# Performance work log

Measured on AMD Instinct MI355X. Metric: run time of the kernel, lower is better.

Reference implementation:

```python
import jax, jax.numpy as jnp
import numpy as np
import math

B, N, DQK, DV, M = 8, 8192, 128, 128, 256


def _make_omega(m: int, d: int, seed: int = 0) -> jnp.ndarray:
    """Block-orthogonal random feature matrix, shape [d, m] (matches torch _omega)."""
    rng = np.random.default_rng(seed)
    blocks = []
    nblocks = m // d
    for _ in range(nblocks):
        q, _ = np.linalg.qr(rng.standard_normal((d, d)))
        blocks.append(q.T)
    missing = m - nblocks * d
    if missing > 0:
        q, _ = np.linalg.qr(rng.standard_normal((d, d)))
        blocks.append(q.T[:missing])
    norm = np.linalg.norm(rng.standard_normal((m, d)), axis=1, keepdims=True)
    omega = (norm * np.vstack(blocks)).T  # [d, m]
    return jnp.asarray(omega, dtype=jnp.float32)


def setup_inputs() -> dict:
    key = jax.random.key(0)
    kq, kk, kv = jax.random.split(key, 3)
    Q = jax.random.normal(kq, (B, N, DQK), jnp.float32)
    K = jax.random.normal(kk, (B, N, DQK), jnp.float32)
    V = jax.random.normal(kv, (B, N, DV), jnp.float32)
    atom_mask = jnp.ones((B, N), jnp.float32)
    omega = _make_omega(M, DQK)
    return {"Q": Q, "K": K, "V": V, "atom_mask": atom_mask, "omega": omega}


def _phi(X, mask, omega, is_query: bool, eps: float = 1e-4):
    """Project into random-feature space with Performer stabilization."""
    d = X.shape[-1]
    m = omega.shape[-1]
    U = (X / d ** 0.25) @ omega                       # [B, N, m]
    h = jnp.sum(X * X, axis=-1, keepdims=True) / (2.0 * d ** 0.5)
    if is_query:
        mx = jnp.max(U, axis=-1, keepdims=True)       # per-token max
    else:
        mx = jnp.max(U, axis=(-2, -1), keepdims=True)  # per-batch max
    return (jnp.exp(U - h - mx) + eps) / math.sqrt(m) * mask[..., None]


def reference(Q, K, V, atom_mask, omega):
    eps = 1e-8
    Qp = _phi(Q, atom_mask, omega, True)   # [B, N, M]
    Kp = _phi(K, atom_mask, omega, False)  # [B, N, M]
    # norm_n = Qp_n . sum_j Kp_j
    norm = jnp.einsum('bnm,bm->bn', Qp, jnp.sum(Kp, axis=1))[..., None] + eps
    KV = jnp.einsum('bnm,bnv->bmv', Kp, V)             # [B, M, DV]
    return jnp.einsum('bnm,bmv->bnv', Qp, KV) / norm   # [B, N, DV]
```

## Files before the change

kernel.cpp:

```cpp
#include <hip/hip_runtime.h>
#include <math.h>

#define BB 8
#define NN 8192
#define DD 128
#define MM 256
#define DVV 128
#define PP 32
#define CHUNK 32

#define XSCALE 0.29730177875068026f
#define INV_SQRT_M 0.0625f

typedef _Float16 f16x8 __attribute__((ext_vector_type(8)));
typedef float f32x16 __attribute__((ext_vector_type(16)));

#define FR(s, l) ((s) * 520 + (l) * 8)

__device__ __forceinline__ unsigned f2ord(float f) {
    unsigned u = __float_as_uint(f);
    return (u & 0x80000000u) ? ~u : (u | 0x80000000u);
}
__device__ __forceinline__ float ord2f(unsigned u) {
    return (u & 0x80000000u) ? __uint_as_float(u & 0x7fffffffu) : __uint_as_float(~u);
}
__device__ __forceinline__ f32x16 mfma16(f16x8 a, f16x8 b, f32x16 c) {
    return __builtin_amdgcn_mfma_f32_32x32x16_f16(a, b, c, 0, 0, 0);
}
__device__ __forceinline__ int rowf(int r, int q) { return (r & 3) + 8 * (r >> 2) + 4 * q; }

__device__ __forceinline__ void stage_A(const float* __restrict__ src,
                                        _Float16* R1, float* hs, float* msk,
                                        const float* __restrict__ mrow, bool do_h) {
    const int tid = threadIdx.x;
    const int t = tid >> 3, ks = tid & 7;
    const float4* s4 = (const float4*)(src + t * DD + ks * 16);
    float x[16];
    #pragma unroll
    for (int u = 0; u < 4; ++u) {
        float4 v = s4[u];
        x[u*4+0] = v.x * XSCALE; x[u*4+1] = v.y * XSCALE;
        x[u*4+2] = v.z * XSCALE; x[u*4+3] = v.w * XSCALE;
    }
    if (do_h) {
        float p = 0.f;
        #pragma unroll
        for (int u = 0; u < 16; ++u) p += x[u] * x[u];
        p += __shfl_xor(p, 1, 64); p += __shfl_xor(p, 2, 64); p += __shfl_xor(p, 4, 64);
        if (ks == 0) { hs[t] = 0.5f * p; msk[t] = mrow[t]; }
    }
    #pragma unroll
    for (int q = 0; q < 2; ++q) {
        f16x8 h8, l8;
        #pragma unroll
        for (int j = 0; j < 8; ++j) {
            float xv = x[q*8 + j];
            _Float16 h = (_Float16)xv;
            h8[j] = h; l8[j] = (_Float16)(xv - (float)h);
        }
        *(f16x8*)&R1[FR(0*8 + ks, q*32 + t)] = h8;
        *(f16x8*)&R1[FR(1*8 + ks, q*32 + t)] = l8;
    }
}

__device__ __forceinline__ void stage_BV(const float* __restrict__ src, _Float16* R1) {
    const int tid = threadIdx.x;
    const int t = tid >> 3, c0 = (tid & 7) * 16;
    const int ts = t >> 4, qq = (t >> 3) & 1, j = t & 7;
    const float4* s4 = (const float4*)(src + t * DVV + c0);
    #pragma unroll
    for (int u = 0; u < 4; ++u) {
        float4 v = s4[u];
        float vv[4] = {v.x, v.y, v.z, v.w};
        #pragma unroll
        for (int e = 0; e < 4; ++e) {
            int c = c0 + u*4 + e;
            int vt = c >> 5, iv = c & 31;
            _Float16 h = (_Float16)vv[e];
            R1[FR((0*4 + vt)*2 + ts, qq*32 + iv) + j] = h;
            R1[FR((1*4 + vt)*2 + ts, qq*32 + iv) + j] = (_Float16)(vv[e] - (float)h);
        }
    }
}

__global__ __launch_bounds__(256) void pack_kernel(const float* __restrict__ omega,
                                                   _Float16* __restrict__ omh,
                                                   _Float16* __restrict__ oml,
                                                   unsigned* __restrict__ kmaxord) {
    int g = blockIdx.x * 256 + threadIdx.x;
    if (g < BB) kmaxord[g] = f2ord(-INFINITY);
    int lane = g & 63, ks = (g >> 6) & 7, nt = g >> 9;
    int q = lane >> 5, i = lane & 31;
    f16x8 h8, l8;
    #pragma unroll
    for (int j = 0; j < 8; ++j) {
        float w = omega[(size_t)(ks*16 + q*8 + j) * MM + nt*32 + i];
        _Float16 h = (_Float16)w;
        h8[j] = h; l8[j] = (_Float16)(w - (float)h);
    }
    ((f16x8*)omh)[g] = h8;
    ((f16x8*)oml)[g] = l8;
}

__global__ __launch_bounds__(256) void kmax_kernel(const float* __restrict__ K,
                                                   const _Float16* __restrict__ omh,
                                                   unsigned* __restrict__ kmaxord) {
    __shared__ __align__(16) _Float16 R1[16 * 520];
    __shared__ float wred[4];
    const int b = blockIdx.y;
    const int tid = threadIdx.x, w = tid >> 6, lane = tid & 63;
    const int w2 = 2 * w;
    const f16x8* OH = (const f16x8*)omh;

    float mx = -INFINITY;
    #pragma unroll 1
    for (int c = 0; c < 2; ++c) {
        int t0 = (blockIdx.x * 2 + c) * CHUNK;
        __syncthreads();
        stage_A(K + ((size_t)b*NN + t0) * DD, R1, nullptr, nullptr, nullptr, false);
        __syncthreads();
        f32x16 a0, a1;
        #pragma unroll
        for (int r = 0; r < 16; ++r) { a0[r] = 0.f; a1[r] = 0.f; }
        f16x8 X0 = OH[(w2*8 + 0)*64 + lane];
        f16x8 X1 = OH[((w2+1)*8 + 0)*64 + lane];
        #pragma unroll 1
        for (int ks = 0; ks < 8; ks += 2) {
            f16x8 Y0 = OH[(w2*8 + ks + 1)*64 + lane];
            f16x8 Y1 = OH[((w2+1)*8 + ks + 1)*64 + lane];
            f16x8 ah = *(const f16x8*)&R1[FR(ks, lane)];
            a0 = mfma16(ah, X0, a0);
            a1 = mfma16(ah, X1, a1);
            int k2 = (ks + 2) & 7;
            X0 = OH[(w2*8 + k2)*64 + lane];
            X1 = OH[((w2+1)*8 + k2)*64 + lane];
            f16x8 ah2 = *(const f16x8*)&R1[FR(ks + 1, lane)];
            a0 = mfma16(ah2, Y0, a0);
            a1 = mfma16(ah2, Y1, a1);
        }
        #pragma unroll
        for (int r = 0; r < 16; ++r) mx = fmaxf(mx, fmaxf(a0[r], a1[r]));
    }
    #pragma unroll
    for (int off = 1; off < 64; off <<= 1) mx = fmaxf(mx, __shfl_xor(mx, off, 64));
    if (lane == 0) wred[w] = mx;
    __syncthreads();
    if (tid == 0)
        atomicMax(kmaxord + b,
                  f2ord(fmaxf(fmaxf(wred[0], wred[1]), fmaxf(wred[2], wred[3]))));
}

__global__ __launch_bounds__(256) void kv_kernel(const float* __restrict__ K,
                                                 const float* __restrict__ V,
                                                 const float* __restrict__ mask,
                                                 const _Float16* __restrict__ omh,
                                                 const _Float16* __restrict__ oml,
                                                 const unsigned* __restrict__ kmaxord,
                                                 float* __restrict__ pkv,
                                                 float* __restrict__ pks) {
    __shared__ __align__(16) _Float16 R1[16 * 520];
    __shared__ __align__(16) _Float16 R2[16 * 520];
    __shared__ float hs[32], msk[32];
    const int b = blockIdx.y, bx = blockIdx.x;
    const int rest = bx >> 3;
    const int h = rest & 1;
    const int p = (rest >> 1) * 8 + (bx & 7);
    const int tid = threadIdx.x, w = tid >> 6, lane = tid & 63;
    const int i = tid & 31, q = (tid >> 5) & 1;
    const int nt = h * 4 + w;
    const float kmaxv = ord2f(kmaxord[b]);
    const f16x8* OH = (const f16x8*)omh;
    const f16x8* OL = (const f16x8*)oml;

    f32x16 kvacc[4];
    #pragma unroll
    for (int vt = 0; vt < 4; ++vt)
        #pragma unroll
        for (int r = 0; r < 16; ++r) kvacc[vt][r] = 0.f;
    float ksa = 0.f;

    #pragma unroll 1
    for (int c = 0; c < 8; ++c) {
        int t0 = (p * 8 + c) * CHUNK;
        __syncthreads();
        stage_A(K + ((size_t)b*NN + t0) * DD, R1, hs, msk,
                mask + (size_t)b*NN + t0, true);
        __syncthreads();

        f32x16 a0;
        #pragma unroll
        for (int r = 0; r < 16; ++r) a0[r] = 0.f;
        f16x8 Xh = OH[(nt*8 + 0)*64 + lane];
        f16x8 Xl = OL[(nt*8 + 0)*64 + lane];
        #pragma unroll 1
        for (int ks = 0; ks < 8; ks += 2) {
            f16x8 Yh = OH[(nt*8 + ks + 1)*64 + lane];
            f16x8 Yl = OL[(nt*8 + ks + 1)*64 + lane];
            f16x8 ah = *(const f16x8*)&R1[FR(ks, lane)];
            f16x8 al = *(const f16x8*)&R1[FR(8 + ks, lane)];
            a0 = mfma16(ah, Xh, a0);
            a0 = mfma16(ah, Xl, a0);
            a0 = mfma16(al, Xh, a0);
            int k2 = (ks + 2) & 7;
            Xh = OH[(nt*8 + k2)*64 + lane];
            Xl = OL[(nt*8 + k2)*64 + lane];
            f16x8 ah2 = *(const f16x8*)&R1[FR(ks + 1, lane)];
            f16x8 al2 = *(const f16x8*)&R1[FR(8 + ks + 1, lane)];
            a0 = mfma16(ah2, Yh, a0);
            a0 = mfma16(ah2, Yl, a0);
            a0 = mfma16(al2, Yh, a0);
        }
        __syncthreads();

        stage_BV(V + ((size_t)b*NN + t0) * DVV, R1);
        #pragma unroll
        for (int r = 0; r < 16; ++r) {
            int tok = rowf(r, q);
            float hh = hs[tok] + kmaxv;
            float mm = msk[tok] * INV_SQRT_M;
            float kp = (__expf(a0[r] - hh) + 1e-4f) * mm;
            ksa += kp;
            int ts = tok >> 4, qq = (tok >> 3) & 1, j = tok & 7;
            _Float16 hv = (_Float16)kp;
            R2[FR(w*2 + ts, qq*32 + i) + j] = hv;
            R2[FR(8 + w*2 + ts, qq*32 + i) + j] = (_Float16)(kp - (float)hv);
        }
        __syncthreads();

        f16x8 ah2[2], al2[2];
        #pragma unroll
        for (int ts = 0; ts < 2; ++ts) {
            ah2[ts] = *(const f16x8*)&R2[FR(w*2 + ts, lane)];
            al2[ts] = *(const f16x8*)&R2[FR(8 + w*2 + ts, lane)];
        }
        #pragma unroll
        for (int vt = 0; vt < 4; ++vt) {
            #pragma unroll
            for (int ts = 0; ts < 2; ++ts) {
                f16x8 bh = *(const f16x8*)&R1[FR(vt*2 + ts, lane)];
                f16x8 bl = *(const f16x8*)&R1[FR(8 + vt*2 + ts, lane)];
                kvacc[vt] = mfma16(ah2[ts], bh, kvacc[vt]);
                kvacc[vt] = mfma16(ah2[ts], bl, kvacc[vt]);
                kvacc[vt] = mfma16(al2[ts], bh, kvacc[vt]);
            }
        }
    }

    float* dst = pkv + ((size_t)(b * PP + p) << 15);
    #pragma unroll
    for (int vt = 0; vt < 4; ++vt)
        #pragma unroll
        for (int r = 0; r < 16; ++r) {
            int feat = nt*32 + rowf(r, q);
            dst[feat * DVV + vt*32 + i] = kvacc[vt][r];
        }
    {
        float s = ksa + __shfl_xor(ksa, 32, 64);
        if (q == 0) pks[(size_t)(b * PP + p) * MM + nt*32 + i] = s;
    }
}

__global__ __launch_bounds__(256) void reduce_kernel(const float* __restrict__ pkv,
                                                     const float* __restrict__ pks,
                                                     float* __restrict__ ksum,
                                                     _Float16* __restrict__ kvph,
                                                     _Float16* __restrict__ kvpl) {
    const int b = blockIdx.y;
    int g = blockIdx.x * 256 + threadIdx.x;
    float s = 0.f;
    for (int p = 0; p < PP; ++p) s += pkv[((size_t)(b * PP + p) << 15) + g];
    int f = g >> 7, v = g & 127;
    int vt = v >> 5, iv = v & 31, fs = f >> 4, qq = (f >> 3) & 1, j = f & 7;
    size_t idx = (size_t)b * 32768 + (size_t)((vt*16 + fs)*64 + qq*32 + iv)*8 + j;
    _Float16 h = (_Float16)s;
    kvph[idx] = h;
    kvpl[idx] = (_Float16)(s - (float)h);
    if (blockIdx.x == 0) {
        float ss = 0.f;
        for (int p = 0; p < PP; ++p) ss += pks[(size_t)(b * PP + p) * MM + g];
        ksum[b * MM + g] = ss;
    }
}

__global__ __launch_bounds__(256) void out_kernel(const float* __restrict__ Q,
                                                  const float* __restrict__ mask,
                                                  const _Float16* __restrict__ omh,
                                                  const _Float16* __restrict__ oml,
                                                  const float* __restrict__ ksum,
                                                  const _Float16* __restrict__ kvph,
                                                  const _Float16* __restrict__ kvpl,
                                                  float* __restrict__ out) {
    __shared__ __align__(16) _Float16 R2[32 * 520];
    __shared__ float hs[32], msk[32], wmax[4][32], norms[32];
    const int b = blockIdx.y;
    const int tid = threadIdx.x, w = tid >> 6, lane = tid & 63;
    const int i = tid & 31, q = (tid >> 5) & 1;
    const int w2 = 2 * w;
    const f16x8* OH = (const f16x8*)omh;
    const f16x8* OL = (const f16x8*)oml;
    const f16x8* KH = (const f16x8*)kvph + (size_t)b * 4096 + (w*16)*64 + lane;
    const f16x8* KL = (const f16x8*)kvpl + (size_t)b * 4096 + (w*16)*64 + lane;
    const float nk0 = ksum[b * MM + w2*32 + i];
    const float nk1 = ksum[b * MM + (w2+1)*32 + i];

    #pragma unroll 1
    for (int c = 0; c < 2; ++c) {
        int t0 = (blockIdx.x * 2 + c) * CHUNK;
        __syncthreads();
        stage_A(Q + ((size_t)b*NN + t0) * DD, R2, hs, msk,
                mask + (size_t)b*NN + t0, true);
        if (tid < 32) norms[tid] = 1e-8f;
        __syncthreads();

        f32x16 a0, a1;
        #pragma unroll
        for (int r = 0; r < 16; ++r) { a0[r] = 0.f; a1[r] = 0.f; }
        f16x8 X0h = OH[(w2*8 + 0)*64 + lane], X0l = OL[(w2*8 + 0)*64 + lane];
        f16x8 X1h = OH[((w2+1)*8 + 0)*64 + lane], X1l = OL[((w2+1)*8 + 0)*64 + lane];
        #pragma unroll 1
        for (int ks = 0; ks < 8; ks += 2) {
            f16x8 Y0h = OH[(w2*8 + ks + 1)*64 + lane], Y0l = OL[(w2*8 + ks + 1)*64 + lane];
            f16x8 Y1h = OH[((w2+1)*8 + ks + 1)*64 + lane], Y1l = OL[((w2+1)*8 + ks + 1)*64 + lane];
            f16x8 ah = *(const f16x8*)&R2[FR(ks, lane)];
            f16x8 al = *(const f16x8*)&R2[FR(8 + ks, lane)];
            a0 = mfma16(ah, X0h, a0); a0 = mfma16(ah, X0l, a0); a0 = mfma16(al, X0h, a0);
            a1 = mfma16(ah, X1h, a1); a1 = mfma16(ah, X1l, a1); a1 = mfma16(al, X1h, a1);
            int k2 = (ks + 2) & 7;
            X0h = OH[(w2*8 + k2)*64 + lane]; X0l = OL[(w2*8 + k2)*64 + lane];
            X1h = OH[((w2+1)*8 + k2)*64 + lane]; X1l = OL[((w2+1)*8 + k2)*64 + lane];
            f16x8 ah2 = *(const f16x8*)&R2[FR(ks + 1, lane)];
            f16x8 al2 = *(const f16x8*)&R2[FR(8 + ks + 1, lane)];
            a0 = mfma16(ah2, Y0h, a0); a0 = mfma16(ah2, Y0l, a0); a0 = mfma16(al2, Y0h, a0);
            a1 = mfma16(ah2, Y1h, a1); a1 = mfma16(ah2, Y1l, a1); a1 = mfma16(al2, Y1h, a1);
        }

        float tm[16];
        #pragma unroll
        for (int r = 0; r < 16; ++r) tm[r] = fmaxf(a0[r], a1[r]);
        #pragma unroll
        for (int off = 1; off < 32; off <<= 1)
            #pragma unroll
            for (int r = 0; r < 16; ++r) tm[r] = fmaxf(tm[r], __shfl_xor(tm[r], off, 64));
        if (i == 0)
            #pragma unroll
            for (int r = 0; r < 16; ++r) wmax[w][rowf(r, q)] = tm[r];
        __syncthreads();

        float nacc[16];
        #pragma unroll
        for (int r = 0; r < 16; ++r) {
            int tok = rowf(r, q);
            float tmax = fmaxf(fmaxf(wmax[0][tok], wmax[1][tok]),
                               fmaxf(wmax[2][tok], wmax[3][tok]));
            float hh = hs[tok] + tmax;
            float mm = msk[tok] * INV_SQRT_M;
            float qp0 = (__expf(a0[r] - hh) + 1e-4f) * mm;
            float qp1 = (__expf(a1[r] - hh) + 1e-4f) * mm;
            nacc[r] = qp0 * nk0 + qp1 * nk1;
            {
                int feat = w2*32 + i;
                int fstep = feat >> 4, fq = (i >> 3) & 1, fj = i & 7;
                _Float16 hv = (_Float16)qp0;
                R2[FR(fstep, fq*32 + tok) + fj] = hv;
                R2[FR(16 + fstep, fq*32 + tok) + fj] = (_Float16)(qp0 - (float)hv);
            }
            {
                int feat = (w2+1)*32 + i;
                int fstep = feat >> 4, fq = (i >> 3) & 1, fj = i & 7;
                _Float16 hv = (_Float16)qp1;
                R2[FR(fstep, fq*32 + tok) + fj] = hv;
                R2[FR(16 + fstep, fq*32 + tok) + fj] = (_Float16)(qp1 - (float)hv);
            }
        }
        #pragma unroll
        for (int off = 1; off < 32; off <<= 1)
            #pragma unroll
            for (int r = 0; r < 16; ++r) nacc[r] += __shfl_xor(nacc[r], off, 64);
        if (i == 0)
            #pragma unroll
            for (int r = 0; r < 16; ++r) atomicAdd(&norms[rowf(r, q)], nacc[r]);
        __syncthreads();

        f32x16 oa;
        #pragma unroll
        for (int r = 0; r < 16; ++r) oa[r] = 0.f;
        f16x8 Fh = KH[0], Fl = KL[0];
        #pragma unroll 1
        for (int fs = 0; fs < 16; fs += 2) {
            f16x8 Gh = KH[(fs + 1)*64], Gl = KL[(fs + 1)*64];
            f16x8 ah = *(const f16x8*)&R2[FR(fs, lane)];
            f16x8 al = *(const f16x8*)&R2[FR(16 + fs, lane)];
            oa = mfma16(ah, Fh, oa); oa = mfma16(ah, Fl, oa); oa = mfma16(al, Fh, oa);
            int f2 = (fs + 2) & 15;
            Fh = KH[f2*64]; Fl = KL[f2*64];
            f16x8 ah2 = *(const f16x8*)&R2[FR(fs + 1, lane)];
            f16x8 al2 = *(const f16x8*)&R2[FR(16 + fs + 1, lane)];
            oa = mfma16(ah2, Gh, oa); oa = mfma16(ah2, Gl, oa); oa = mfma16(al2, Gh, oa);
        }

        float* ob = out + ((size_t)b*NN + t0) * DVV + w*32 + i;
        #pragma unroll
        for (int r = 0; r < 16; ++r) {
            int tok = rowf(r, q);
            ob[(size_t)tok * DVV] = oa[r] * __builtin_amdgcn_rcpf(norms[tok]);
        }
    }
}

extern "C" void kernel_launch(void* const* d_in, const int* in_sizes, int n_in,
                              void* d_out, int out_size, void* d_ws, size_t ws_size,
                              hipStream_t stream) {
    const float* Q     = (const float*)d_in[0];
    const float* K     = (const float*)d_in[1];
    const float* V     = (const float*)d_in[2];
    const float* mask  = (const float*)d_in[3];
    const float* omega = (const float*)d_in[4];
    float* out = (float*)d_out;

    char* ws = (char*)d_ws;
    _Float16* omh    = (_Float16*)(ws);
    _Float16* oml    = (_Float16*)(ws + (64 << 10));
    unsigned* kmaxord = (unsigned*)(ws + (128 << 10));
    float*    ksum   = (float*)(ws + (132 << 10));
    float*    pks    = (float*)(ws + (140 << 10));
    _Float16* kvph   = (_Float16*)(ws + (400 << 10));
    _Float16* kvpl   = (_Float16*)(ws + (912 << 10));
    float*    pkv    = (float*)(ws + (2 << 20));

    pack_kernel<<<16, 256, 0, stream>>>(omega, omh, oml, kmaxord);
    kmax_kernel<<<dim3(128, BB), 256, 0, stream>>>(K, omh, kmaxord);
    kv_kernel<<<dim3(64, BB), 256, 0, stream>>>(K, V, mask, omh, oml, kmaxord, pkv, pks);
    reduce_kernel<<<dim3(128, BB), 256, 0, stream>>>(pkv, pks, ksum, kvph, kvpl);
    out_kernel<<<dim3(128, BB), 256, 0, stream>>>(Q, mask, omh, oml, ksum, kvph, kvpl, out);
}
```

Before: 250.8 us.

## Software-pipeline kv and out kernels with register prefetch and double-buffered LDS

The kv kernel now prefetches the next chunk's K, V and mask into registers while computing the current chunk. It overlaps the previous chunk's KV MFMA accumulation with the current projection, using double-buffered V tiles and h/mask arrays. The out kernel is restructured the same way: the next chunk's Q is prefetched, the previous chunk's PV product is interleaved with the current projection, and norm atomics are replaced by per-wave shared partials. The grid is halved so each block handles four chunks, and the inner loops are fully unrolled. The changes aim to hide global load latency and cut barriers, at the cost of more LDS and register pressure, which may lower occupancy.

```diff
diff --git a/kernel.cpp b/kernel.cpp
--- a/kernel.cpp
+++ b/kernel.cpp
@@ -29,57 +29,55 @@
 }
 __device__ __forceinline__ int rowf(int r, int q) { return (r & 3) + 8 * (r >> 2) + 4 * q; }
 
-__device__ __forceinline__ void stage_A(const float* __restrict__ src,
-                                        _Float16* R1, float* hs, float* msk,
-                                        const float* __restrict__ mrow, bool do_h) {
+__device__ __forceinline__ void loadX16(const float* __restrict__ src, float x[16]) {
+    const int tid = threadIdx.x;
+    const float4* s4 = (const float4*)(src + (tid >> 3) * 128 + (tid & 7) * 16);
+    #pragma unroll
+    for (int u = 0; u < 4; ++u) {
+        float4 v = s4[u];
+        x[u*4+0] = v.x; x[u*4+1] = v.y; x[u*4+2] = v.z; x[u*4+3] = v.w;
+    }
+}
+
+__device__ __forceinline__ void writeA(const float xin[16], _Float16* R1,
+                                       float* hs, float* msk, float mv, bool do_h) {
     const int tid = threadIdx.x;
     const int t = tid >> 3, ks = tid & 7;
-    const float4* s4 = (const float4*)(src + t * DD + ks * 16);
     float x[16];
     #pragma unroll
-    for (int u = 0; u < 4; ++u) {
-        float4 v = s4[u];
-        x[u*4+0] = v.x * XSCALE; x[u*4+1] = v.y * XSCALE;
-        x[u*4+2] = v.z * XSCALE; x[u*4+3] = v.w * XSCALE;
-    }
+    for (int u = 0; u < 16; ++u) x[u] = xin[u] * XSCALE;
     if (do_h) {
         float p = 0.f;
         #pragma unroll
         for (int u = 0; u < 16; ++u) p += x[u] * x[u];
         p += __shfl_xor(p, 1, 64); p += __shfl_xor(p, 2, 64); p += __shfl_xor(p, 4, 64);
-        if (ks == 0) { hs[t] = 0.5f * p; msk[t] = mrow[t]; }
-    }
-    #pragma unroll
-    for (int q = 0; q < 2; ++q) {
+        if (ks == 0) { hs[t] = 0.5f * p; msk[t] = mv; }
+    }
+    #pragma unroll
+    for (int qq = 0; qq < 2; ++qq) {
         f16x8 h8, l8;
         #pragma unroll
         for (int j = 0; j < 8; ++j) {
-            float xv = x[q*8 + j];
+            float xv = x[qq*8 + j];
             _Float16 h = (_Float16)xv;
             h8[j] = h; l8[j] = (_Float16)(xv - (float)h);
         }
-        *(f16x8*)&R1[FR(0*8 + ks, q*32 + t)] = h8;
-        *(f16x8*)&R1[FR(1*8 + ks, q*32 + t)] = l8;
-    }
-}
-
-__device__ __forceinline__ void stage_BV(const float* __restrict__ src, _Float16* R1) {
+        *(f16x8*)&R1[FR(0*8 + ks, qq*32 + t)] = h8;
+        *(f16x8*)&R1[FR(1*8 + ks, qq*32 + t)] = l8;
+    }
+}
+
+__device__ __forceinline__ void writeV(const float xin[16], _Float16* RV) {
     const int tid = threadIdx.x;
     const int t = tid >> 3, c0 = (tid & 7) * 16;
     const int ts = t >> 4, qq = (t >> 3) & 1, j = t & 7;
-    const float4* s4 = (const float4*)(src + t * DVV + c0);
-    #pragma unroll
-    for (int u = 0; u < 4; ++u) {
-        float4 v = s4[u];
-        float vv[4] = {v.x, v.y, v.z, v.w};
-        #pragma unroll
-        for (int e = 0; e < 4; ++e) {
-            int c = c0 + u*4 + e;
-            int vt = c >> 5, iv = c & 31;
-            _Float16 h = (_Float16)vv[e];
-            R1[FR((0*4 + vt)*2 + ts, qq*32 + iv) + j] = h;
-            R1[FR((1*4 + vt)*2 + ts, qq*32 + iv) + j] = (_Float16)(vv[e] - (float)h);
-        }
+    #pragma unroll
+    for (int u = 0; u < 16; ++u) {
+        int c = c0 + u;
+        int vt = c >> 5, iv = c & 31;
+        _Float16 h = (_Float16)xin[u];
+        RV[FR((0*4 + vt)*2 + ts, qq*32 + iv) + j] = h;
+        RV[FR((1*4 + vt)*2 + ts, qq*32 + iv) + j] = (_Float16)(xin[u] - (float)h);
     }
 }
 
@@ -117,26 +115,25 @@
     for (int c = 0; c < 2; ++c) {
         int t0 = (blockIdx.x * 2 + c) * CHUNK;
         __syncthreads();
-        stage_A(K + ((size_t)b*NN + t0) * DD, R1, nullptr, nullptr, nullptr, false);
+        {
+            float xk[16];
+            loadX16(K + ((size_t)b*NN + t0) * DD, xk);
+            writeA(xk, R1, nullptr, nullptr, 0.f, false);
+        }
         __syncthreads();
         f32x16 a0, a1;
         #pragma unroll
         for (int r = 0; r < 16; ++r) { a0[r] = 0.f; a1[r] = 0.f; }
         f16x8 X0 = OH[(w2*8 + 0)*64 + lane];
         f16x8 X1 = OH[((w2+1)*8 + 0)*64 + lane];
-        #pragma unroll 1
-        for (int ks = 0; ks < 8; ks += 2) {
-            f16x8 Y0 = OH[(w2*8 + ks + 1)*64 + lane];
-            f16x8 Y1 = OH[((w2+1)*8 + ks + 1)*64 + lane];
+        #pragma unroll
+        for (int ks = 0; ks < 8; ++ks) {
+            f16x8 Y0, Y1;
+            if (ks < 7) { Y0 = OH[(w2*8 + ks + 1)*64 + lane]; Y1 = OH[((w2+1)*8 + ks + 1)*64 + lane]; }
             f16x8 ah = *(const f16x8*)&R1[FR(ks, lane)];
             a0 = mfma16(ah, X0, a0);
             a1 = mfma16(ah, X1, a1);
-            int k2 = (ks + 2) & 7;
-            X0 = OH[(w2*8 + k2)*64 + lane];
-            X1 = OH[((w2+1)*8 + k2)*64 + lane];
-            f16x8 ah2 = *(const f16x8*)&R1[FR(ks + 1, lane)];
-            a0 = mfma16(ah2, Y0, a0);
-            a1 = mfma16(ah2, Y1, a1);
+            X0 = Y0; X1 = Y1;
         }
         #pragma unroll
         for (int r = 0; r < 16; ++r) mx = fmaxf(mx, fmaxf(a0[r], a1[r]));
@@ -160,7 +157,9 @@
                                                  float* __restrict__ pks) {
     __shared__ __align__(16) _Float16 R1[16 * 520];
     __shared__ __align__(16) _Float16 R2[16 * 520];
-    __shared__ float hs[32], msk[32];
+    __shared__ __align__(16) _Float16 RV0[16 * 520];
+    __shared__ __align__(16) _Float16 RV1[16 * 520];
+    __shared__ float hs[2][32], msk[2][32];
     const int b = blockIdx.y, bx = blockIdx.x;
     const int rest = bx >> 3;
     const int h = rest & 1;
@@ -168,9 +167,13 @@
     const int tid = threadIdx.x, w = tid >> 6, lane = tid & 63;
     const int i = tid & 31, q = (tid >> 5) & 1;
     const int nt = h * 4 + w;
+    const int tld = tid >> 3;
     const float kmaxv = ord2f(kmaxord[b]);
     const f16x8* OH = (const f16x8*)omh;
     const f16x8* OL = (const f16x8*)oml;
+    const float* Kb = K + (size_t)b * NN * DD;
+    const float* Vb = V + (size_t)b * NN * DVV;
+    const float* Mb = mask + (size_t)b * NN;
 
     f32x16 kvacc[4];
     #pragma unroll
@@ -179,46 +182,77 @@
         for (int r = 0; r < 16; ++r) kvacc[vt][r] = 0.f;
     float ksa = 0.f;
 
+    {
+        int t0 = p * 8 * CHUNK;
+        float xk[16], xv[16];
+        loadX16(Kb + (size_t)t0 * DD, xk);
+        loadX16(Vb + (size_t)t0 * DVV, xv);
+        float mv = Mb[t0 + tld];
+        writeA(xk, R1, hs[0], msk[0], mv, true);
+        writeV(xv, RV0);
+    }
+    __syncthreads();
+
     #pragma unroll 1
-    for (int c = 0; c < 8; ++c) {
-        int t0 = (p * 8 + c) * CHUNK;
-        __syncthreads();
-        stage_A(K + ((size_t)b*NN + t0) * DD, R1, hs, msk,
-                mask + (size_t)b*NN + t0, true);
-        __syncthreads();
-
-        f32x16 a0;
-        #pragma unroll
-        for (int r = 0; r < 16; ++r) a0[r] = 0.f;
+    for (int t = 0; t < 8; ++t) {
+        const bool pre = (t + 1 < 8);
+        float xk[16], xv[16], mv = 0.f;
+        if (pre) {
+            int t1 = (p * 8 + t + 1) * CHUNK;
+            loadX16(Kb + (size_t)t1 * DD, xk);
+            loadX16(Vb + (size_t)t1 * DVV, xv);
+            mv = Mb[t1 + tld];
+        }
+        _Float16* RVprev = (t & 1) ? RV0 : RV1;
+
+        f32x16 a0a, a0b;
+        #pragma unroll
+        for (int r = 0; r < 16; ++r) { a0a[r] = 0.f; a0b[r] = 0.f; }
+        f16x8 kh0, kl0, kh1, kl1;
+        if (t > 0) {
+            kh0 = *(const f16x8*)&R2[FR(w*2 + 0, lane)];
+            kl0 = *(const f16x8*)&R2[FR(8 + w*2 + 0, lane)];
+            kh1 = *(const f16x8*)&R2[FR(w*2 + 1, lane)];
+            kl1 = *(const f16x8*)&R2[FR(8 + w*2 + 1, lane)];
+        }
         f16x8 Xh = OH[(nt*8 + 0)*64 + lane];
         f16x8 Xl = OL[(nt*8 + 0)*64 + lane];
-        #pragma unroll 1
-        for (int ks = 0; ks < 8; ks += 2) {
-            f16x8 Yh = OH[(nt*8 + ks + 1)*64 + lane];
-            f16x8 Yl = OL[(nt*8 + ks + 1)*64 + lane];
-            f16x8 ah = *(const f16x8*)&R1[FR(ks, lane)];
-            f16x8 al = *(const f16x8*)&R1[FR(8 + ks, lane)];
-            a0 = mfma16(ah, Xh, a0);
-            a0 = mfma16(ah, Xl, a0);
-            a0 = mfma16(al, Xh, a0);
-            int k2 = (ks + 2) & 7;
-            Xh = OH[(nt*8 + k2)*64 + lane];
-            Xl = OL[(nt*8 + k2)*64 + lane];
-            f16x8 ah2 = *(const f16x8*)&R1[FR(ks + 1, lane)];
-            f16x8 al2 = *(const f16x8*)&R1[FR(8 + ks + 1, lane)];
-            a0 = mfma16(ah2, Yh, a0);
-            a0 = mfma16(ah2, Yl, a0);
-            a0 = mfma16(al2, Yh, a0);
+        #pragma unroll
+        for (int s = 0; s < 8; ++s) {
+            f16x8 Yh, Yl;
+            if (s < 7) { Yh = OH[(nt*8 + s + 1)*64 + lane]; Yl = OL[(nt*8 + s + 1)*64 + lane]; }
+            f16x8 ah = *(const f16x8*)&R1[FR(s, lane)];
+            f16x8 al = *(const f16x8*)&R1[FR(8 + s, lane)];
+            if (s & 1) {
+                a0b = mfma16(ah, Xh, a0b); a0b = mfma16(ah, Xl, a0b); a0b = mfma16(al, Xh, a0b);
+            } else {
+                a0a = mfma16(ah, Xh, a0a); a0a = mfma16(ah, Xl, a0a); a0a = mfma16(al, Xh, a0a);
+            }
+            if (t > 0) {
+                const int vt = s >> 1, ts = s & 1;
+                f16x8 kh = ts ? kh1 : kh0, kl = ts ? kl1 : kl0;
+                f16x8 bh = *(const f16x8*)&RVprev[FR(vt*2 + ts, lane)];
+                f16x8 bl = *(const f16x8*)&RVprev[FR(8 + vt*2 + ts, lane)];
+                kvacc[vt] = mfma16(kh, bh, kvacc[vt]);
+                kvacc[vt] = mfma16(kh, bl, kvacc[vt]);
+                kvacc[vt] = mfma16(kl, bh, kvacc[vt]);
+            }
+            Xh = Yh; Xl = Yl;
         }
         __syncthreads();
 
-        stage_BV(V + ((size_t)b*NN + t0) * DVV, R1);
+        if (pre) {
+            writeA(xk, R1, hs[(t+1)&1], msk[(t+1)&1], mv, true);
+            writeV(xv, RVprev);
+        }
+        const float* hsv = hs[t & 1];
+        const float* mskv = msk[t & 1];
         #pragma unroll
         for (int r = 0; r < 16; ++r) {
             int tok = rowf(r, q);
-            float hh = hs[tok] + kmaxv;
-            float mm = msk[tok] * INV_SQRT_M;
-            float kp = (__expf(a0[r] - hh) + 1e-4f) * mm;
+            float hh = hsv[tok] + kmaxv;
+            float mm = mskv[tok] * INV_SQRT_M;
+            float kp = (__expf((a0a[r] + a0b[r]) - hh) + 1e-4f) * mm;
             ksa += kp;
             int ts = tok >> 4, qq = (tok >> 3) & 1, j = tok & 7;
             _Float16 hv = (_Float16)kp;
@@ -226,22 +260,23 @@
             R2[FR(8 + w*2 + ts, qq*32 + i) + j] = (_Float16)(kp - (float)hv);
         }
         __syncthreads();
-
-        f16x8 ah2[2], al2[2];
-        #pragma unroll
-        for (int ts = 0; ts < 2; ++ts) {
-            ah2[ts] = *(const f16x8*)&R2[FR(w*2 + ts, lane)];
-            al2[ts] = *(const f16x8*)&R2[FR(8 + w*2 + ts, lane)];
-        }
+    }
+
+    {
+        f16x8 kh0 = *(const f16x8*)&R2[FR(w*2 + 0, lane)];
+        f16x8 kl0 = *(const f16x8*)&R2[FR(8 + w*2 + 0, lane)];
+        f16x8 kh1 = *(const f16x8*)&R2[FR(w*2 + 1, lane)];
+        f16x8 kl1 = *(const f16x8*)&R2[FR(8 + w*2 + 1, lane)];
         #pragma unroll
         for (int vt = 0; vt < 4; ++vt) {
             #pragma unroll
             for (int ts = 0; ts < 2; ++ts) {
-                f16x8 bh = *(const f16x8*)&R1[FR(vt*2 + ts, lane)];
-                f16x8 bl = *(const f16x8*)&R1[FR(8 + vt*2 + ts, lane)];
-                kvacc[vt] = mfma16(ah2[ts], bh, kvacc[vt]);
-                kvacc[vt] = mfma16(ah2[ts], bl, kvacc[vt]);
-                kvacc[vt] = mfma16(al2[ts], bh, kvacc[vt]);
+                f16x8 kh = ts ? kh1 : kh0, kl = ts ? kl1 : kl0;
+                f16x8 bh = *(const f16x8*)&RV1[FR(vt*2 + ts, lane)];
+                f16x8 bl = *(const f16x8*)&RV1[FR(8 + vt*2 + ts, lane)];
+                kvacc[vt] = mfma16(kh, bh, kvacc[vt]);
+                kvacc[vt] = mfma16(kh, bl, kvacc[vt]);
+                kvacc[vt] = mfma16(kl, bh, kvacc[vt]);
             }
         }
     }
@@ -290,120 +325,151 @@
                                                   const _Float16* __restrict__ kvph,
                                                   const _Float16* __restrict__ kvpl,
                                                   float* __restrict__ out) {
+    __shared__ __align__(16) _Float16 R1[16 * 520];
     __shared__ __align__(16) _Float16 R2[32 * 520];
-    __shared__ float hs[32], msk[32], wmax[4][32], norms[32];
+    __shared__ float hs[2][32], msk[2][32], wmax[4][32], nws[2][4][32];
     const int b = blockIdx.y;
     const int tid = threadIdx.x, w = tid >> 6, lane = tid & 63;
     const int i = tid & 31, q = (tid >> 5) & 1;
     const int w2 = 2 * w;
+    const int tld = tid >> 3;
     const f16x8* OH = (const f16x8*)omh;
     const f16x8* OL = (const f16x8*)oml;
     const f16x8* KH = (const f16x8*)kvph + (size_t)b * 4096 + (w*16)*64 + lane;
     const f16x8* KL = (const f16x8*)kvpl + (size_t)b * 4096 + (w*16)*64 + lane;
     const float nk0 = ksum[b * MM + w2*32 + i];
     const float nk1 = ksum[b * MM + (w2+1)*32 + i];
+    const float* Qb = Q + (size_t)b * NN * DD;
+    const float* Mb = mask + (size_t)b * NN;
+    const int base = blockIdx.x * 4;
+
+    {
+        float xq[16];
+        loadX16(Qb + (size_t)(base * CHUNK) * DD, xq);
+        float mv = Mb[base * CHUNK + tld];
+        writeA(xq, R1, hs[0], msk[0], mv, true);
+    }
+    __syncthreads();
 
     #pragma unroll 1
-    for (int c = 0; c < 2; ++c) {
-        int t0 = (blockIdx.x * 2 + c) * CHUNK;
+    for (int c = 0; c < 5; ++c) {
+        const bool doU  = (c < 4);
+        const bool doPV = (c > 0);
+        const bool pre  = (c + 1 < 4);
+        float xq[16], mv = 0.f;
+        if (pre) {
+            int t1 = (base + c + 1) * CHUNK;
+            loadX16(Qb + (size_t)t1 * DD, xq);
+            mv = Mb[t1 + tld];
+        }
+
+        f32x16 a0, a1, oa, ob;
+        #pragma unroll
+        for (int r = 0; r < 16; ++r) { a0[r] = 0.f; a1[r] = 0.f; oa[r] = 0.f; ob[r] = 0.f; }
+        f16x8 X0h, X0l, X1h, X1l, F0h, F0l, F1h, F1l;
+        if (doU) {
+            X0h = OH[(w2*8 + 0)*64 + lane];     X0l = OL[(w2*8 + 0)*64 + lane];
+            X1h = OH[((w2+1)*8 + 0)*64 + lane]; X1l = OL[((w2+1)*8 + 0)*64 + lane];
+        }
+        if (doPV) {
+            F0h = KH[0*64]; F0l = KL[0*64];
+            F1h = KH[1*64]; F1l = KL[1*64];
+        }
+        #pragma unroll
+        for (int s = 0; s < 8; ++s) {
+            f16x8 Y0h, Y0l, Y1h, Y1l, G0h, G0l, G1h, G1l;
+            if (s < 7) {
+                if (doU) {
+                    Y0h = OH[(w2*8 + s + 1)*64 + lane];     Y0l = OL[(w2*8 + s + 1)*64 + lane];
+                    Y1h = OH[((w2+1)*8 + s + 1)*64 + lane]; Y1l = OL[((w2+1)*8 + s + 1)*64 + lane];
+                }
+                if (doPV) {
+                    G0h = KH[(2*s + 2)*64]; G0l = KL[(2*s + 2)*64];
+                    G1h = KH[(2*s + 3)*64]; G1l = KL[(2*s + 3)*64];
+                }
+            }
+            if (doU) {
+                f16x8 ah = *(const f16x8*)&R1[FR(s, lane)];
+                f16x8 al = *(const f16x8*)&R1[FR(8 + s, lane)];
+                a0 = mfma16(ah, X0h, a0); a0 = mfma16(ah, X0l, a0); a0 = mfma16(al, X0h, a0);
+                a1 = mfma16(ah, X1h, a1); a1 = mfma16(ah, X1l, a1); a1 = mfma16(al, X1h, a1);
+            }
+            if (doPV) {
+                f16x8 ph0 = *(const f16x8*)&R2[FR(2*s, lane)];
+                f16x8 pl0 = *(const f16x8*)&R2[FR(16 + 2*s, lane)];
+                oa = mfma16(ph0, F0h, oa); oa = mfma16(ph0, F0l, oa); oa = mfma16(pl0, F0h, oa);
+                f16x8 ph1 = *(const f16x8*)&R2[FR(2*s + 1, lane)];
+                f16x8 pl1 = *(const f16x8*)&R2[FR(16 + 2*s + 1, lane)];
+                ob = mfma16(ph1, F1h, ob); ob = mfma16(ph1, F1l, ob); ob = mfma16(pl1, F1h, ob);
+            }
+            X0h = Y0h; X0l = Y0l; X1h = Y1h; X1l = Y1l;
+            F0h = G0h; F0l = G0l; F1h = G1h; F1l = G1l;
+        }
+
+        if (doPV) {
+            const int pb = (c - 1) & 1;
+            int tp = (base + c - 1) * CHUNK;
+            float* obp = out + ((size_t)b*NN + tp) * DVV + w*32 + i;
+            #pragma unroll
+            for (int r = 0; r < 16; ++r) {
+                int tok = rowf(r, q);
+                float nrm = nws[pb][0][tok] + nws[pb][1][tok]
+                          + nws[pb][2][tok] + nws[pb][3][tok] + 1e-8f;
+                obp[(size_t)tok * DVV] = (oa[r] + ob[r]) * __builtin_amdgcn_rcpf(nrm);
+            }
+        }
+
+        if (doU) {
+            float tm[16];
+            #pragma unroll
+            for (int r = 0; r < 16; ++r) tm[r] = fmaxf(a0[r], a1[r]);
+            #pragma unroll
+            for (int off = 1; off < 32; off <<= 1)
+                #pragma unroll
+                for (int r = 0; r < 16; ++r) tm[r] = fmaxf(tm[r], __shfl_xor(tm[r], off, 64));
+            if (i == 0)
+                #pragma unroll
+                for (int r = 0; r < 16; ++r) wmax[w][rowf(r, q)] = tm[r];
+        }
         __syncthreads();
-        stage_A(Q + ((size_t)b*NN + t0) * DD, R2, hs, msk,
-                mask + (size_t)b*NN + t0, true);
-        if (tid < 32) norms[tid] = 1e-8f;
+
+        if (pre) writeA(xq, R1, hs[(c+1)&1], msk[(c+1)&1], mv, true);
+        if (doU) {
+            const float* hsv = hs[c & 1];
+            const float* mskv = msk[c & 1];
+            float nacc[16];
+            #pragma unroll
+            for (int r = 0; r < 16; ++r) {
+                int tok = rowf(r, q);
+                float tmax = fmaxf(fmaxf(wmax[0][tok], wmax[1][tok]),
+                                   fmaxf(wmax[2][tok], wmax[3][tok]));
+                float hh = hsv[tok] + tmax;
+                float mm = mskv[tok] * INV_SQRT_M;
+                float qp0 = (__expf(a0[r] - hh) + 1e-4f) * mm;
+                float qp1 = (__expf(a1[r] - hh) + 1e-4f) * mm;
+                nacc[r] = qp0 * nk0 + qp1 * nk1;
+                {
+                    int fstep = (w2*32 + i) >> 4, fq = (i >> 3) & 1, fj = i & 7;
+                    _Float16 hv = (_Float16)qp0;
+                    R2[FR(fstep, fq*32 + tok) + fj] = hv;
+                    R2[FR(16 + fstep, fq*32 + tok) + fj] = (_Float16)(qp0 - (float)hv);
+                }
+                {
+                    int fstep = ((w2+1)*32 + i) >> 4, fq = (i >> 3) & 1, fj = i & 7;
+                    _Float16 hv = (_Float16)qp1;
+                    R2[FR(fstep, fq*32 + tok) + fj] = hv;
+                    R2[FR(16 + fstep, fq*32 + tok) + fj] = (_Float16)(qp1 - (float)hv);
+                }
+            }
+            #pragma unroll
+            for (int off = 1; off < 32; off <<= 1)
+                #pragma unroll
+                for (int r = 0; r < 16; ++r) nacc[r] += __shfl_xor(nacc[r], off, 64);
+            if (i == 0)
+                #pragma unroll
+                for (int r = 0; r < 16; ++r) nws[c & 1][w][rowf(r, q)] = nacc[r];
+        }
         __syncthreads();
-
-        f32x16 a0, a1;
-        #pragma unroll
-        for (int r = 0; r < 16; ++r) { a0[r] = 0.f; a1[r] = 0.f; }
-        f16x8 X0h = OH[(w2*8 + 0)*64 + lane], X0l = OL[(w2*8 + 0)*64 + lane];
-        f16x8 X1h = OH[((w2+1)*8 + 0)*64 + lane], X1l = OL[((w2+1)*8 + 0)*64 + lane];
-        #pragma unroll 1
-        for (int ks = 0; ks < 8; ks += 2) {
-            f16x8 Y0h = OH[(w2*8 + ks + 1)*64 + lane], Y0l = OL[(w2*8 + ks + 1)*64 + lane];
-            f16x8 Y1h = OH[((w2+1)*8 + ks + 1)*64 + lane], Y1l = OL[((w2+1)*8 + ks + 1)*64 + lane];
-            f16x8 ah = *(const f16x8*)&R2[FR(ks, lane)];
-            f16x8 al = *(const f16x8*)&R2[FR(8 + ks, lane)];
-            a0 = mfma16(ah, X0h, a0); a0 = mfma16(ah, X0l, a0); a0 = mfma16(al, X0h, a0);
-            a1 = mfma16(ah, X1h, a1); a1 = mfma16(ah, X1l, a1); a1 = mfma16(al, X1h, a1);
-            int k2 = (ks + 2) & 7;
-            X0h = OH[(w2*8 + k2)*64 + lane]; X0l = OL[(w2*8 + k2)*64 + lane];
-            X1h = OH[((w2+1)*8 + k2)*64 + lane]; X1l = OL[((w2+1)*8 + k2)*64 + lane];
-            f16x8 ah2 = *(const f16x8*)&R2[FR(ks + 1, lane)];
-            f16x8 al2 = *(const f16x8*)&R2[FR(8 + ks + 1, lane)];
-            a0 = mfma16(ah2, Y0h, a0); a0 = mfma16(ah2, Y0l, a0); a0 = mfma16(al2, Y0h, a0);
-            a1 = mfma16(ah2, Y1h, a1); a1 = mfma16(ah2, Y1l, a1); a1 = mfma16(al2, Y1h, a1);
-        }
-
-        float tm[16];
-        #pragma unroll
-        for (int r = 0; r < 16; ++r) tm[r] = fmaxf(a0[r], a1[r]);
-        #pragma unroll
-        for (int off = 1; off < 32; off <<= 1)
-            #pragma unroll
-            for (int r = 0; r < 16; ++r) tm[r] = fmaxf(tm[r], __shfl_xor(tm[r], off, 64));
-        if (i == 0)
-            #pragma unroll
-            for (int r = 0; r < 16; ++r) wmax[w][rowf(r, q)] = tm[r];
-        __syncthreads();
-
-        float nacc[16];
-        #pragma unroll
-        for (int r = 0; r < 16; ++r) {
-            int tok = rowf(r, q);
-            float tmax = fmaxf(fmaxf(wmax[0][tok], wmax[1][tok]),
-                               fmaxf(wmax[2][tok], wmax[3][tok]));
-            float hh = hs[tok] + tmax;
-            float mm = msk[tok] * INV_SQRT_M;
-            float qp0 = (__expf(a0[r] - hh) + 1e-4f) * mm;
-            float qp1 = (__expf(a1[r] - hh) + 1e-4f) * mm;
-            nacc[r] = qp0 * nk0 + qp1 * nk1;
-            {
-                int feat = w2*32 + i;
-                int fstep = feat >> 4, fq = (i >> 3) & 1, fj = i & 7;
-                _Float16 hv = (_Float16)qp0;
-                R2[FR(fstep, fq*32 + tok) + fj] = hv;
-                R2[FR(16 + fstep, fq*32 + tok) + fj] = (_Float16)(qp0 - (float)hv);
-            }
-            {
-                int feat = (w2+1)*32 + i;
-                int fstep = feat >> 4, fq = (i >> 3) & 1, fj = i & 7;
-                _Float16 hv = (_Float16)qp1;
-                R2[FR(fstep, fq*32 + tok) + fj] = hv;
-                R2[FR(16 + fstep, fq*32 + tok) + fj] = (_Float16)(qp1 - (float)hv);
-            }
-        }
-        #pragma unroll
-        for (int off = 1; off < 32; off <<= 1)
-            #pragma unroll
-            for (int r = 0; r < 16; ++r) nacc[r] += __shfl_xor(nacc[r], off, 64);
-        if (i == 0)
-            #pragma unroll
-            for (int r = 0; r < 16; ++r) atomicAdd(&norms[rowf(r, q)], nacc[r]);
-        __syncthreads();
-
-        f32x16 oa;
-        #pragma unroll
-        for (int r = 0; r < 16; ++r) oa[r] = 0.f;
-        f16x8 Fh = KH[0], Fl = KL[0];
-        #pragma unroll 1
-        for (int fs = 0; fs < 16; fs += 2) {
-            f16x8 Gh = KH[(fs + 1)*64], Gl = KL[(fs + 1)*64];
-            f16x8 ah = *(const f16x8*)&R2[FR(fs, lane)];
-            f16x8 al = *(const f16x8*)&R2[FR(16 + fs, lane)];
-            oa = mfma16(ah, Fh, oa); oa = mfma16(ah, Fl, oa); oa = mfma16(al, Fh, oa);
-            int f2 = (fs + 2) & 15;
-            Fh = KH[f2*64]; Fl = KL[f2*64];
-            f16x8 ah2 = *(const f16x8*)&R2[FR(fs + 1, lane)];
-            f16x8 al2 = *(const f16x8*)&R2[FR(16 + fs + 1, lane)];
-            oa = mfma16(ah2, Gh, oa); oa = mfma16(ah2, Gl, oa); oa = mfma16(al2, Gh, oa);
-        }
-
-        float* ob = out + ((size_t)b*NN + t0) * DVV + w*32 + i;
-        #pragma unroll
-        for (int r = 0; r < 16; ++r) {
-            int tok = rowf(r, q);
-            ob[(size_t)tok * DVV] = oa[r] * __builtin_amdgcn_rcpf(norms[tok]);
-        }
     }
 }
 
@@ -431,5 +497,5 @@
     kmax_kernel<<<dim3(128, BB), 256, 0, stream>>>(K, omh, kmaxord);
     kv_kernel<<<dim3(64, BB), 256, 0, stream>>>(K, V, mask, omh, oml, kmaxord, pkv, pks);
     reduce_kernel<<<dim3(128, BB), 256, 0, stream>>>(pkv, pks, ksum, kvph, kvpl);
-    out_kernel<<<dim3(128, BB), 256, 0, stream>>>(Q, mask, omh, oml, ksum, kvph, kvpl, out);
-}
+    out_kernel<<<dim3(64, BB), 256, 0, stream>>>(Q, mask, omh, oml, ksum, kvph, kvpl, out);
+}
```

After: 263.8 us. 5.2% more time.
